# Kernel optimization log

Hardware: AMD Instinct MI355X
Metric: run time of the kernel (lower is better)

Reference implementation:

```python
import jax, jax.numpy as jnp
import numpy as np

INPUT_LEN = 24
HIDDEN = 64
BATCH = 8192


def _lstm_layer(seq, Wih, Whh, bih, bhh):
    """Single torch-style LSTM layer. seq: [T, B, in] -> hs: [T, B, H].
    Gate order matches torch: i, f, g, o."""
    B = seq.shape[1]
    H = Whh.shape[1]
    b = bih + bhh
    h0 = jnp.zeros((B, H), seq.dtype)
    c0 = jnp.zeros((B, H), seq.dtype)

    def step(carry, x_t):
        h, c = carry
        gates = x_t @ Wih.T + h @ Whh.T + b  # [B, 4H]
        i, f, g, o = jnp.split(gates, 4, axis=-1)
        c = jax.nn.sigmoid(f) * c + jax.nn.sigmoid(i) * jnp.tanh(g)
        h = jax.nn.sigmoid(o) * jnp.tanh(c)
        return (h, c), h

    _, hs = jax.lax.scan(step, (h0, c0), seq)
    return hs


def setup_inputs() -> dict:
    key = jax.random.key(0)
    ks = jax.random.split(key, 16)
    H = HIDDEN
    s = 1.0 / np.sqrt(H)  # torch LSTM/Linear init scale
    u = lambda k, shape, sc: jax.random.uniform(k, shape, jnp.float32, -sc, sc)
    return {
        "x": jax.random.normal(ks[0], (BATCH, INPUT_LEN), jnp.float32),
        # LSTM layer 0 (input size 1)
        "Wih0": u(ks[1], (4 * H, 1), s),
        "Whh0": u(ks[2], (4 * H, H), s),
        "bih0": u(ks[3], (4 * H,), s),
        "bhh0": u(ks[4], (4 * H,), s),
        # LSTM layer 1 (input size H)
        "Wih1": u(ks[5], (4 * H, H), s),
        "Whh1": u(ks[6], (4 * H, H), s),
        "bih1": u(ks[7], (4 * H,), s),
        "bhh1": u(ks[8], (4 * H,), s),
        # predictor MLP: Linear(H,32) -> ReLU -> Linear(32,1)
        "W1": u(ks[9], (32, H), s),
        "b1": u(ks[10], (32,), s),
        "W2": u(ks[11], (1, 32), 1.0 / np.sqrt(32)),
        "b2": u(ks[12], (1,), 1.0 / np.sqrt(32)),
        "damping": jnp.asarray(0.1, jnp.float32),
        "steps": 20,
    }


def reference(x, Wih0, Whh0, bih0, bhh0, Wih1, Whh1, bih1, bhh1,
              W1, b1, W2, b2, damping, steps):
    cur = x[..., None]  # [B, T, 1]
    alpha = jax.nn.sigmoid(damping)
    preds = []
    prev = None
    for _ in range(steps):
        seq = jnp.transpose(cur, (1, 0, 2))  # [T, B, 1]
        h1 = _lstm_layer(seq, Wih0, Whh0, bih0, bhh0)   # [T, B, H]
        h2 = _lstm_layer(h1, Wih1, Whh1, bih1, bhh1)     # [T, B, H]
        last = h2[-1]                                     # [B, H]
        pred = jax.nn.relu(last @ W1.T + b1) @ W2.T + b2  # [B, 1]
        if prev is not None:
            # torch: pred*(1-alpha) + predictions[-1].detach()*alpha*0.5
            pred = pred * (1.0 - alpha) + jax.lax.stop_gradient(prev) * alpha * 0.5
        preds.append(pred)
        prev = pred
        cur = jnp.concatenate([cur[:, 1:, :], pred[:, None, :]], axis=1)
    return jnp.concatenate(preds, axis=1)  # [B, steps]
```

## Files before the change

### kernel.cpp

```cpp
#include <hip/hip_runtime.h>


typedef _Float16 f16x8 __attribute__((ext_vector_type(8)));
typedef float f32x4 __attribute__((ext_vector_type(4)));

#define NBLK 512
#define NTHR 256
#define SRB  144

__device__ __forceinline__ float rcp_(float x) { return __builtin_amdgcn_rcpf(x); }
__device__ __forceinline__ float exp2_(float x) { return __builtin_amdgcn_exp2f(x); }
__device__ __forceinline__ f32x4 mfma16(uint4 a, uint4 b, f32x4 c) {
  return __builtin_amdgcn_mfma_f32_16x16x32_f16(
      __builtin_bit_cast(f16x8, a), __builtin_bit_cast(f16x8, b), c, 0, 0, 0);
}
__device__ __forceinline__ uint4 pack8s(const float* p, float s) {
  union { uint4 u; _Float16 h[8]; } r;
  #pragma unroll
  for (int i = 0; i < 8; ++i) r.h[i] = (_Float16)(p[i] * s);
  return r.u;
}
__device__ __forceinline__ float gatestep(float aI, float aF, float aG, float aO,
                                          float& cst) {
  float xx = exp2_(-aI), xf = exp2_(-aF), yy = exp2_(-aG), xo = exp2_(-aO);
  float P = (1.0f + xx) * (1.0f + yy);
  float Q = 1.0f + xf;
  float N = fmaf(cst, P, (1.0f - yy) * Q);
  float cv = N * rcp_(P * Q);
  cst = cv;
  float z = exp2_(-2.88539008178f * cv);
  return (1.0f - z) * rcp_((1.0f + xo) * (1.0f + z));
}

__global__ __launch_bounds__(NTHR, 2) void lstm_forecast(
    const float* __restrict__ x,
    const float* __restrict__ Wih0, const float* __restrict__ Whh0,
    const float* __restrict__ bih0, const float* __restrict__ bhh0,
    const float* __restrict__ Wih1, const float* __restrict__ Whh1,
    const float* __restrict__ bih1, const float* __restrict__ bhh1,
    const float* __restrict__ W1,   const float* __restrict__ b1,
    const float* __restrict__ W2,   const float* __restrict__ b2,
    const float* __restrict__ damping, const int* __restrict__ stepsPtr,
    float* __restrict__ out)
{
  __shared__ __align__(16) char h1s[2][16 * SRB];
  __shared__ __align__(16) char h2s[2][16 * SRB];
  __shared__ __align__(16) float win[24 * 16];
  __shared__ __align__(16) float pm[2][16];

  const int tid  = threadIdx.x;
  const int wave = tid >> 6;
  const int lane = tid & 63;
  const int cc   = lane & 15;
  const int hi   = lane >> 4;
  const int b0g  = blockIdx.x * 16;
  const float L2E = 1.44269504089f;

  uint4 wB0[4][2], wB1[4][2], wB2[4][2];
  float bias0v[4], wih0v[4];
  f32x4 bi1[4];
  #pragma unroll
  for (int gt = 0; gt < 4; ++gt) {
    float sc = (gt == 2) ? 2.0f * L2E : L2E;
    int row = (wave + 4 * gt) * 16 + cc;
    #pragma unroll
    for (int f = 0; f < 2; ++f) {
      int col = f * 32 + hi * 8;
      wB0[gt][f] = pack8s(Whh0 + row * 64 + col, sc);
      wB1[gt][f] = pack8s(Wih1 + row * 64 + col, sc);
      wB2[gt][f] = pack8s(Whh1 + row * 64 + col, sc);
    }
    bias0v[gt] = (bih0[row] + bhh0[row]) * sc;
    wih0v[gt]  = Wih0[row] * sc;
    float b1c  = (bih1[row] + bhh1[row]) * sc;
    #pragma unroll
    for (int r = 0; r < 4; ++r) bi1[gt][r] = b1c;
  }
  uint4 wM[2];
  {
    int row = (wave & 1) * 16 + cc;
    wM[0] = pack8s(W1 + row * 64 + hi * 8, 1.0f);
    wM[1] = pack8s(W1 + row * 64 + 32 + hi * 8, 1.0f);
  }
  const float w2v  = W2[(wave & 1) * 16 + cc];
  const float b1vv = b1[(wave & 1) * 16 + cc];
  const float alpha  = rcp_(1.0f + exp2_(-L2E * damping[0]));
  const int   nsteps = stepsPtr[0];
  const float b2v    = b2[0];

  for (int e = tid; e < 384; e += NTHR) {
    int b = e & 15, t = e >> 4;
    win[t * 16 + b] = x[(b0g + b) * 24 + t];
  }
  __syncthreads();

  const int offA = cc * SRB + hi * 16;
  const int offS = (wave * 16 + cc) * 2;
  float prevp = 0.0f;

  for (int s = 0; s < nsteps; ++s) {
    float c1[4] = {0, 0, 0, 0}, c2s[4] = {0, 0, 0, 0};

    {
      float4 xw = *(const float4*)&win[(s % 24) * 16 + hi * 4];
      float xa[4] = {xw.x, xw.y, xw.z, xw.w};
      #pragma unroll
      for (int r = 0; r < 4; ++r) {
        float hv = gatestep(fmaf(xa[r], wih0v[0], bias0v[0]),
                            fmaf(xa[r], wih0v[1], bias0v[1]),
                            fmaf(xa[r], wih0v[2], bias0v[2]),
                            fmaf(xa[r], wih0v[3], bias0v[3]), c1[r]);
        *(_Float16*)(h1s[0] + (hi * 4 + r) * SRB + offS) = (_Float16)hv;
      }
    }
    __syncthreads();
    uint4 a1lo = *(const uint4*)(h1s[0] + offA);
    uint4 a1hi = *(const uint4*)(h1s[0] + offA + 64);
    uint4 a2lo = make_uint4(0, 0, 0, 0), a2hi = make_uint4(0, 0, 0, 0);

    for (int t = 0; t < 23; ++t) {
      int pb = (t + 1) & 1;
      int ph = s + t + 1; if (ph >= 24) ph -= 24;
      float4 xw = *(const float4*)&win[ph * 16 + hi * 4];
      float xa[4] = {xw.x, xw.y, xw.z, xw.w};

      f32x4 acc1[4], acc0[4];
      #pragma unroll
      for (int gt = 0; gt < 4; ++gt) {
        f32x4 tv = mfma16(a1lo, wB1[gt][0], bi1[gt]);
        tv = mfma16(a1hi, wB1[gt][1], tv);
        tv = mfma16(a2lo, wB2[gt][0], tv);
        acc1[gt] = mfma16(a2hi, wB2[gt][1], tv);
      }
      #pragma unroll
      for (int gt = 0; gt < 4; ++gt) {
        f32x4 ai;
        #pragma unroll
        for (int r = 0; r < 4; ++r) ai[r] = fmaf(xa[r], wih0v[gt], bias0v[gt]);
        f32x4 tv = mfma16(a1lo, wB0[gt][0], ai);
        acc0[gt] = mfma16(a1hi, wB0[gt][1], tv);
      }

      char* h2d = h2s[pb];
      char* h1d = h1s[pb];
      #pragma unroll
      for (int r = 0; r < 4; ++r) {
        float hv = gatestep(acc1[0][r], acc1[1][r], acc1[2][r], acc1[3][r], c2s[r]);
        *(_Float16*)(h2d + (hi * 4 + r) * SRB + offS) = (_Float16)hv;
      }
      #pragma unroll
      for (int r = 0; r < 4; ++r) {
        float hv = gatestep(acc0[0][r], acc0[1][r], acc0[2][r], acc0[3][r], c1[r]);
        *(_Float16*)(h1d + (hi * 4 + r) * SRB + offS) = (_Float16)hv;
      }
      __syncthreads();
      a1lo = *(const uint4*)(h1s[pb] + offA);
      a1hi = *(const uint4*)(h1s[pb] + offA + 64);
      a2lo = *(const uint4*)(h2s[pb] + offA);
      a2hi = *(const uint4*)(h2s[pb] + offA + 64);
    }

    {
      f32x4 acc1[4];
      #pragma unroll
      for (int gt = 0; gt < 4; ++gt) {
        f32x4 tv = mfma16(a1lo, wB1[gt][0], bi1[gt]);
        tv = mfma16(a1hi, wB1[gt][1], tv);
        tv = mfma16(a2lo, wB2[gt][0], tv);
        acc1[gt] = mfma16(a2hi, wB2[gt][1], tv);
      }
      #pragma unroll
      for (int r = 0; r < 4; ++r) {
        float cv = c2s[r];
        float hv = gatestep(acc1[0][r], acc1[1][r], acc1[2][r], acc1[3][r], cv);
        *(_Float16*)(h2s[0] + (hi * 4 + r) * SRB + offS) = (_Float16)hv;
      }
    }
    __syncthreads();

    if (wave < 2) {
      uint4 hflo = *(const uint4*)(h2s[0] + offA);
      uint4 hfhi = *(const uint4*)(h2s[0] + offA + 64);
      f32x4 am;
      #pragma unroll
      for (int r = 0; r < 4; ++r) am[r] = b1vv;
      am = mfma16(hflo, wM[0], am);
      am = mfma16(hfhi, wM[1], am);
      float yp[4];
      #pragma unroll
      for (int r = 0; r < 4; ++r) yp[r] = fmaxf(am[r], 0.0f) * w2v;
      #pragma unroll
      for (int mask = 1; mask <= 8; mask <<= 1) {
        #pragma unroll
        for (int r = 0; r < 4; ++r) yp[r] += __shfl_xor(yp[r], mask);
      }
      if (cc == 0) {
        #pragma unroll
        for (int r = 0; r < 4; ++r) pm[wave][hi * 4 + r] = yp[r];
      }
    }
    __syncthreads();

    if (wave == 0 && lane < 16) {
      float y = pm[0][lane] + pm[1][lane] + b2v;
      float pd = (s == 0) ? y : fmaf(y, 1.0f - alpha, prevp * (alpha * 0.5f));
      prevp = pd;
      win[(s % 24) * 16 + lane] = pd;
      out[(long)(b0g + lane) * nsteps + s] = pd;
    }
    __syncthreads();
  }
}

extern "C" void kernel_launch(void* const* d_in, const int* in_sizes, int n_in,
                              void* d_out, int out_size, void* d_ws, size_t ws_size,
                              hipStream_t stream) {
  (void)in_sizes; (void)n_in; (void)out_size; (void)d_ws; (void)ws_size;
  lstm_forecast<<<NBLK, NTHR, 0, stream>>>(
      (const float*)d_in[0],
      (const float*)d_in[1],  (const float*)d_in[2],
      (const float*)d_in[3],  (const float*)d_in[4],
      (const float*)d_in[5],  (const float*)d_in[6],
      (const float*)d_in[7],  (const float*)d_in[8],
      (const float*)d_in[9],  (const float*)d_in[10],
      (const float*)d_in[11], (const float*)d_in[12],
      (const float*)d_in[13], (const int*)d_in[14],
      (float*)d_out);
}
```

Before: 597.0 us.

## Process two interleaved 16-row batch tiles per block to hide MFMA latency

Each block now handles 32 batch rows as two independent 16-row sub-tiles, interleaving their MFMA chains and gate computations inside one recurrence step. Half as many blocks are launched, with launch bounds lowered to one block per CU. The two independent dependency chains are meant to fill MFMA and transcendental latency inside a wave and to halve the barriers per unit of work. The cost is doubled register and LDS use per block and lower occupancy, which could spill registers or leave CUs underused.

```diff
diff --git a/kernel.cpp b/kernel.cpp
--- a/kernel.cpp
+++ b/kernel.cpp
@@ -4,7 +4,7 @@
 typedef _Float16 f16x8 __attribute__((ext_vector_type(8)));
 typedef float f32x4 __attribute__((ext_vector_type(4)));
 
-#define NBLK 512
+#define NBLK 256
 #define NTHR 256
 #define SRB  144
 
@@ -32,7 +32,7 @@
   return (1.0f - z) * rcp_((1.0f + xo) * (1.0f + z));
 }
 
-__global__ __launch_bounds__(NTHR, 2) void lstm_forecast(
+__global__ __launch_bounds__(NTHR, 1) void lstm_forecast(
     const float* __restrict__ x,
     const float* __restrict__ Wih0, const float* __restrict__ Whh0,
     const float* __restrict__ bih0, const float* __restrict__ bhh0,
@@ -43,17 +43,17 @@
     const float* __restrict__ damping, const int* __restrict__ stepsPtr,
     float* __restrict__ out)
 {
-  __shared__ __align__(16) char h1s[2][16 * SRB];
-  __shared__ __align__(16) char h2s[2][16 * SRB];
-  __shared__ __align__(16) float win[24 * 16];
-  __shared__ __align__(16) float pm[2][16];
+  __shared__ __align__(16) char h1s[2][2][16 * SRB];
+  __shared__ __align__(16) char h2s[2][2][16 * SRB];
+  __shared__ __align__(16) float win[2][24 * 16];
+  __shared__ __align__(16) float pm[2][2][16];
 
   const int tid  = threadIdx.x;
   const int wave = tid >> 6;
   const int lane = tid & 63;
   const int cc   = lane & 15;
   const int hi   = lane >> 4;
-  const int b0g  = blockIdx.x * 16;
+  const int b0g  = blockIdx.x * 32;
   const float L2E = 1.44269504089f;
 
   uint4 wB0[4][2], wB1[4][2], wB2[4][2];
@@ -88,99 +88,127 @@
   const int   nsteps = stepsPtr[0];
   const float b2v    = b2[0];
 
-  for (int e = tid; e < 384; e += NTHR) {
-    int b = e & 15, t = e >> 4;
-    win[t * 16 + b] = x[(b0g + b) * 24 + t];
+  for (int e = tid; e < 768; e += NTHR) {
+    int q   = (e >= 384) ? 1 : 0;
+    int rem = e - q * 384;
+    int b   = rem & 15, t = rem >> 4;
+    win[q][t * 16 + b] = x[(b0g + q * 16 + b) * 24 + t];
   }
   __syncthreads();
 
   const int offA = cc * SRB + hi * 16;
   const int offS = (wave * 16 + cc) * 2;
-  float prevp = 0.0f;
+  float prevp[2] = {0.0f, 0.0f};
 
   for (int s = 0; s < nsteps; ++s) {
-    float c1[4] = {0, 0, 0, 0}, c2s[4] = {0, 0, 0, 0};
-
-    {
-      float4 xw = *(const float4*)&win[(s % 24) * 16 + hi * 4];
+    float c1[2][4], c2s[2][4];
+    #pragma unroll
+    for (int q = 0; q < 2; ++q)
+      #pragma unroll
+      for (int r = 0; r < 4; ++r) { c1[q][r] = 0.0f; c2s[q][r] = 0.0f; }
+
+    #pragma unroll
+    for (int q = 0; q < 2; ++q) {
+      float4 xw = *(const float4*)&win[q][(s % 24) * 16 + hi * 4];
       float xa[4] = {xw.x, xw.y, xw.z, xw.w};
       #pragma unroll
       for (int r = 0; r < 4; ++r) {
         float hv = gatestep(fmaf(xa[r], wih0v[0], bias0v[0]),
                             fmaf(xa[r], wih0v[1], bias0v[1]),
                             fmaf(xa[r], wih0v[2], bias0v[2]),
-                            fmaf(xa[r], wih0v[3], bias0v[3]), c1[r]);
-        *(_Float16*)(h1s[0] + (hi * 4 + r) * SRB + offS) = (_Float16)hv;
-      }
-    }
-    __syncthreads();
-    uint4 a1lo = *(const uint4*)(h1s[0] + offA);
-    uint4 a1hi = *(const uint4*)(h1s[0] + offA + 64);
-    uint4 a2lo = make_uint4(0, 0, 0, 0), a2hi = make_uint4(0, 0, 0, 0);
+                            fmaf(xa[r], wih0v[3], bias0v[3]), c1[q][r]);
+        *(_Float16*)(h1s[q][0] + (hi * 4 + r) * SRB + offS) = (_Float16)hv;
+      }
+    }
+    __syncthreads();
+    uint4 a1lo[2], a1hi[2], a2lo[2], a2hi[2];
+    #pragma unroll
+    for (int q = 0; q < 2; ++q) {
+      a1lo[q] = *(const uint4*)(h1s[q][0] + offA);
+      a1hi[q] = *(const uint4*)(h1s[q][0] + offA + 64);
+      a2lo[q] = make_uint4(0, 0, 0, 0);
+      a2hi[q] = make_uint4(0, 0, 0, 0);
+    }
 
     for (int t = 0; t < 23; ++t) {
       int pb = (t + 1) & 1;
       int ph = s + t + 1; if (ph >= 24) ph -= 24;
-      float4 xw = *(const float4*)&win[ph * 16 + hi * 4];
-      float xa[4] = {xw.x, xw.y, xw.z, xw.w};
-
-      f32x4 acc1[4], acc0[4];
+
+      f32x4 acc1[2][4], acc0[2][4];
+      #pragma unroll
+      for (int q = 0; q < 2; ++q) {
+        #pragma unroll
+        for (int gt = 0; gt < 4; ++gt) {
+          f32x4 tv = mfma16(a1lo[q], wB1[gt][0], bi1[gt]);
+          tv = mfma16(a1hi[q], wB1[gt][1], tv);
+          tv = mfma16(a2lo[q], wB2[gt][0], tv);
+          acc1[q][gt] = mfma16(a2hi[q], wB2[gt][1], tv);
+        }
+      }
+      #pragma unroll
+      for (int q = 0; q < 2; ++q) {
+        float4 xw = *(const float4*)&win[q][ph * 16 + hi * 4];
+        float xa[4] = {xw.x, xw.y, xw.z, xw.w};
+        #pragma unroll
+        for (int gt = 0; gt < 4; ++gt) {
+          f32x4 ai;
+          #pragma unroll
+          for (int r = 0; r < 4; ++r) ai[r] = fmaf(xa[r], wih0v[gt], bias0v[gt]);
+          f32x4 tv = mfma16(a1lo[q], wB0[gt][0], ai);
+          acc0[q][gt] = mfma16(a1hi[q], wB0[gt][1], tv);
+        }
+      }
+
+      #pragma unroll
+      for (int q = 0; q < 2; ++q) {
+        char* h2d = h2s[q][pb];
+        char* h1d = h1s[q][pb];
+        #pragma unroll
+        for (int r = 0; r < 4; ++r) {
+          float hv = gatestep(acc1[q][0][r], acc1[q][1][r], acc1[q][2][r],
+                              acc1[q][3][r], c2s[q][r]);
+          *(_Float16*)(h2d + (hi * 4 + r) * SRB + offS) = (_Float16)hv;
+        }
+        #pragma unroll
+        for (int r = 0; r < 4; ++r) {
+          float hv = gatestep(acc0[q][0][r], acc0[q][1][r], acc0[q][2][r],
+                              acc0[q][3][r], c1[q][r]);
+          *(_Float16*)(h1d + (hi * 4 + r) * SRB + offS) = (_Float16)hv;
+        }
+      }
+      __syncthreads();
+      #pragma unroll
+      for (int q = 0; q < 2; ++q) {
+        a1lo[q] = *(const uint4*)(h1s[q][pb] + offA);
+        a1hi[q] = *(const uint4*)(h1s[q][pb] + offA + 64);
+        a2lo[q] = *(const uint4*)(h2s[q][pb] + offA);
+        a2hi[q] = *(const uint4*)(h2s[q][pb] + offA + 64);
+      }
+    }
+
+    #pragma unroll
+    for (int q = 0; q < 2; ++q) {
+      f32x4 acc1[4];
       #pragma unroll
       for (int gt = 0; gt < 4; ++gt) {
-        f32x4 tv = mfma16(a1lo, wB1[gt][0], bi1[gt]);
-        tv = mfma16(a1hi, wB1[gt][1], tv);
-        tv = mfma16(a2lo, wB2[gt][0], tv);
-        acc1[gt] = mfma16(a2hi, wB2[gt][1], tv);
-      }
-      #pragma unroll
-      for (int gt = 0; gt < 4; ++gt) {
-        f32x4 ai;
-        #pragma unroll
-        for (int r = 0; r < 4; ++r) ai[r] = fmaf(xa[r], wih0v[gt], bias0v[gt]);
-        f32x4 tv = mfma16(a1lo, wB0[gt][0], ai);
-        acc0[gt] = mfma16(a1hi, wB0[gt][1], tv);
-      }
-
-      char* h2d = h2s[pb];
-      char* h1d = h1s[pb];
+        f32x4 tv = mfma16(a1lo[q], wB1[gt][0], bi1[gt]);
+        tv = mfma16(a1hi[q], wB1[gt][1], tv);
+        tv = mfma16(a2lo[q], wB2[gt][0], tv);
+        acc1[gt] = mfma16(a2hi[q], wB2[gt][1], tv);
+      }
       #pragma unroll
       for (int r = 0; r < 4; ++r) {
-        float hv = gatestep(acc1[0][r], acc1[1][r], acc1[2][r], acc1[3][r], c2s[r]);
-        *(_Float16*)(h2d + (hi * 4 + r) * SRB + offS) = (_Float16)hv;
-      }
-      #pragma unroll
-      for (int r = 0; r < 4; ++r) {
-        float hv = gatestep(acc0[0][r], acc0[1][r], acc0[2][r], acc0[3][r], c1[r]);
-        *(_Float16*)(h1d + (hi * 4 + r) * SRB + offS) = (_Float16)hv;
-      }
-      __syncthreads();
-      a1lo = *(const uint4*)(h1s[pb] + offA);
-      a1hi = *(const uint4*)(h1s[pb] + offA + 64);
-      a2lo = *(const uint4*)(h2s[pb] + offA);
-      a2hi = *(const uint4*)(h2s[pb] + offA + 64);
-    }
+        float cv = c2s[q][r];
+        float hv = gatestep(acc1[0][r], acc1[1][r], acc1[2][r], acc1[3][r], cv);
+        *(_Float16*)(h2s[q][0] + (hi * 4 + r) * SRB + offS) = (_Float16)hv;
+      }
+    }
+    __syncthreads();
 
     {
-      f32x4 acc1[4];
-      #pragma unroll
-      for (int gt = 0; gt < 4; ++gt) {
-        f32x4 tv = mfma16(a1lo, wB1[gt][0], bi1[gt]);
-        tv = mfma16(a1hi, wB1[gt][1], tv);
-        tv = mfma16(a2lo, wB2[gt][0], tv);
-        acc1[gt] = mfma16(a2hi, wB2[gt][1], tv);
-      }
-      #pragma unroll
-      for (int r = 0; r < 4; ++r) {
-        float cv = c2s[r];
-        float hv = gatestep(acc1[0][r], acc1[1][r], acc1[2][r], acc1[3][r], cv);
-        *(_Float16*)(h2s[0] + (hi * 4 + r) * SRB + offS) = (_Float16)hv;
-      }
-    }
-    __syncthreads();
-
-    if (wave < 2) {
-      uint4 hflo = *(const uint4*)(h2s[0] + offA);
-      uint4 hfhi = *(const uint4*)(h2s[0] + offA + 64);
+      const int tq = wave >> 1;
+      uint4 hflo = *(const uint4*)(h2s[tq][0] + offA);
+      uint4 hfhi = *(const uint4*)(h2s[tq][0] + offA + 64);
       f32x4 am;
       #pragma unroll
       for (int r = 0; r < 4; ++r) am[r] = b1vv;
@@ -196,17 +224,23 @@
       }
       if (cc == 0) {
         #pragma unroll
-        for (int r = 0; r < 4; ++r) pm[wave][hi * 4 + r] = yp[r];
-      }
-    }
-    __syncthreads();
-
-    if (wave == 0 && lane < 16) {
-      float y = pm[0][lane] + pm[1][lane] + b2v;
-      float pd = (s == 0) ? y : fmaf(y, 1.0f - alpha, prevp * (alpha * 0.5f));
-      prevp = pd;
-      win[(s % 24) * 16 + lane] = pd;
-      out[(long)(b0g + lane) * nsteps + s] = pd;
+        for (int r = 0; r < 4; ++r) pm[tq][wave & 1][hi * 4 + r] = yp[r];
+      }
+    }
+    __syncthreads();
+
+    #pragma unroll
+    for (int q = 0; q < 2; ++q) {
+      if (lane < 16) {
+        float y = pm[q][0][lane] + pm[q][1][lane] + b2v;
+        float pd = (s == 0) ? y
+                            : fmaf(y, 1.0f - alpha, prevp[q] * (alpha * 0.5f));
+        prevp[q] = pd;
+        if (wave == 2 * q) {
+          win[q][(s % 24) * 16 + lane] = pd;
+          out[(long)(b0g + q * 16 + lane) * nsteps + s] = pd;
+        }
+      }
     }
     __syncthreads();
   }
```

After: 758.9 us. 1.27x slower.

## Defer MLP prediction head into next step's first timesteps to drop barriers

Applied to the files above, without the earlier changes.

Moves the per-step MLP head (predictor) out of the serial tail and overlaps it with the first LSTM timestep of the next forecast step. The window write and output store happen one timestep later, which removes two block-wide barriers per forecast step. The MLP weights move from registers into shared memory to cut register pressure, at the cost of extra LDS reads. The restructured loop needs a final epilogue for the last prediction, and its correctness depends on the window slot not being read before it is written.

```diff
diff --git a/kernel.cpp b/kernel.cpp
--- a/kernel.cpp
+++ b/kernel.cpp
@@ -47,6 +47,7 @@
   __shared__ __align__(16) char h2s[2][16 * SRB];
   __shared__ __align__(16) float win[24 * 16];
   __shared__ __align__(16) float pm[2][16];
+  __shared__ __align__(16) uint4 wfm[4][64];
 
   const int tid  = threadIdx.x;
   const int wave = tid >> 6;
@@ -76,11 +77,10 @@
     #pragma unroll
     for (int r = 0; r < 4; ++r) bi1[gt][r] = b1c;
   }
-  uint4 wM[2];
-  {
-    int row = (wave & 1) * 16 + cc;
-    wM[0] = pack8s(W1 + row * 64 + hi * 8, 1.0f);
-    wM[1] = pack8s(W1 + row * 64 + 32 + hi * 8, 1.0f);
+  for (int e = tid; e < 256; e += NTHR) {
+    int l = e & 63, f = (e >> 6) & 1, n = e >> 7;
+    wfm[n * 2 + f][l] =
+        pack8s(W1 + (n * 16 + (l & 15)) * 64 + f * 32 + (l >> 4) * 8, 1.0f);
   }
   const float w2v  = W2[(wave & 1) * 16 + cc];
   const float b1vv = b1[(wave & 1) * 16 + cc];
@@ -97,34 +97,119 @@
   const int offA = cc * SRB + hi * 16;
   const int offS = (wave * 16 + cc) * 2;
   float prevp = 0.0f;
+  float c1[4] = {0, 0, 0, 0}, c2s[4] = {0, 0, 0, 0};
+
+  {
+    float4 xw = *(const float4*)&win[0 * 16 + hi * 4];
+    float xa[4] = {xw.x, xw.y, xw.z, xw.w};
+    #pragma unroll
+    for (int r = 0; r < 4; ++r) {
+      float hv = gatestep(fmaf(xa[r], wih0v[0], bias0v[0]),
+                          fmaf(xa[r], wih0v[1], bias0v[1]),
+                          fmaf(xa[r], wih0v[2], bias0v[2]),
+                          fmaf(xa[r], wih0v[3], bias0v[3]), c1[r]);
+      *(_Float16*)(h1s[0] + (hi * 4 + r) * SRB + offS) = (_Float16)hv;
+    }
+  }
+  __syncthreads();
+  uint4 a1lo = *(const uint4*)(h1s[0] + offA);
+  uint4 a1hi = *(const uint4*)(h1s[0] + offA + 64);
+  uint4 a2lo = make_uint4(0, 0, 0, 0), a2hi = make_uint4(0, 0, 0, 0);
+  uint4 hflo = make_uint4(0, 0, 0, 0), hfhi = make_uint4(0, 0, 0, 0);
+
+#define CORE(PH, PB)                                                           \
+  do {                                                                         \
+    f32x4 acc1[4], acc0[4];                                                    \
+    _Pragma("unroll")                                                          \
+    for (int gt = 0; gt < 4; ++gt) {                                           \
+      f32x4 tv = mfma16(a1lo, wB1[gt][0], bi1[gt]);                            \
+      tv = mfma16(a1hi, wB1[gt][1], tv);                                       \
+      tv = mfma16(a2lo, wB2[gt][0], tv);                                       \
+      acc1[gt] = mfma16(a2hi, wB2[gt][1], tv);                                 \
+    }                                                                          \
+    float4 xw = *(const float4*)&win[(PH) * 16 + hi * 4];                      \
+    float xa[4] = {xw.x, xw.y, xw.z, xw.w};                                    \
+    _Pragma("unroll")                                                          \
+    for (int gt = 0; gt < 4; ++gt) {                                           \
+      f32x4 ai;                                                                \
+      _Pragma("unroll")                                                        \
+      for (int r = 0; r < 4; ++r) ai[r] = fmaf(xa[r], wih0v[gt], bias0v[gt]);  \
+      f32x4 tv = mfma16(a1lo, wB0[gt][0], ai);                                 \
+      acc0[gt] = mfma16(a1hi, wB0[gt][1], tv);                                 \
+    }                                                                          \
+    _Pragma("unroll")                                                          \
+    for (int r = 0; r < 4; ++r) {                                              \
+      float hv = gatestep(acc1[0][r], acc1[1][r], acc1[2][r], acc1[3][r],      \
+                          c2s[r]);                                             \
+      *(_Float16*)(h2s[PB] + (hi * 4 + r) * SRB + offS) = (_Float16)hv;        \
+    }                                                                          \
+    _Pragma("unroll")                                                          \
+    for (int r = 0; r < 4; ++r) {                                              \
+      float hv = gatestep(acc0[0][r], acc0[1][r], acc0[2][r], acc0[3][r],      \
+                          c1[r]);                                              \
+      *(_Float16*)(h1s[PB] + (hi * 4 + r) * SRB + offS) = (_Float16)hv;        \
+    }                                                                          \
+  } while (0)
+
+#define LOADFRAGS(PB)                                                          \
+  do {                                                                         \
+    a1lo = *(const uint4*)(h1s[PB] + offA);                                    \
+    a1hi = *(const uint4*)(h1s[PB] + offA + 64);                               \
+    a2lo = *(const uint4*)(h2s[PB] + offA);                                    \
+    a2hi = *(const uint4*)(h2s[PB] + offA + 64);                               \
+  } while (0)
 
   for (int s = 0; s < nsteps; ++s) {
-    float c1[4] = {0, 0, 0, 0}, c2s[4] = {0, 0, 0, 0};
-
     {
-      float4 xw = *(const float4*)&win[(s % 24) * 16 + hi * 4];
-      float xa[4] = {xw.x, xw.y, xw.z, xw.w};
-      #pragma unroll
-      for (int r = 0; r < 4; ++r) {
-        float hv = gatestep(fmaf(xa[r], wih0v[0], bias0v[0]),
-                            fmaf(xa[r], wih0v[1], bias0v[1]),
-                            fmaf(xa[r], wih0v[2], bias0v[2]),
-                            fmaf(xa[r], wih0v[3], bias0v[3]), c1[r]);
-        *(_Float16*)(h1s[0] + (hi * 4 + r) * SRB + offS) = (_Float16)hv;
-      }
-    }
-    __syncthreads();
-    uint4 a1lo = *(const uint4*)(h1s[0] + offA);
-    uint4 a1hi = *(const uint4*)(h1s[0] + offA + 64);
-    uint4 a2lo = make_uint4(0, 0, 0, 0), a2hi = make_uint4(0, 0, 0, 0);
-
-    for (int t = 0; t < 23; ++t) {
+      int ph = s + 1; if (ph >= 24) ph -= 24;
+      CORE(ph, 1);
+      if (s > 0 && wave < 2) {
+        uint4 m0 = wfm[(wave & 1) * 2 + 0][lane];
+        uint4 m1 = wfm[(wave & 1) * 2 + 1][lane];
+        f32x4 am;
+        #pragma unroll
+        for (int r = 0; r < 4; ++r) am[r] = b1vv;
+        am = mfma16(hflo, m0, am);
+        am = mfma16(hfhi, m1, am);
+        float yp[4];
+        #pragma unroll
+        for (int r = 0; r < 4; ++r) yp[r] = fmaxf(am[r], 0.0f) * w2v;
+        #pragma unroll
+        for (int mask = 1; mask <= 8; mask <<= 1) {
+          #pragma unroll
+          for (int r = 0; r < 4; ++r) yp[r] += __shfl_xor(yp[r], mask);
+        }
+        if (cc == 0) {
+          #pragma unroll
+          for (int r = 0; r < 4; ++r) pm[wave][hi * 4 + r] = yp[r];
+        }
+      }
+      __syncthreads();
+      LOADFRAGS(1);
+    }
+    {
+      if (s > 0 && wave == 0 && lane < 16) {
+        float y = pm[0][lane] + pm[1][lane] + b2v;
+        float pd = (s == 1) ? y : fmaf(y, 1.0f - alpha, prevp * (alpha * 0.5f));
+        prevp = pd;
+        int slot = (s - 1) % 24;
+        win[slot * 16 + lane] = pd;
+        out[(long)(b0g + lane) * nsteps + (s - 1)] = pd;
+      }
+      int ph = s + 2; if (ph >= 24) ph -= 24;
+      CORE(ph, 0);
+      __syncthreads();
+      LOADFRAGS(0);
+    }
+    for (int t = 2; t < 23; ++t) {
       int pb = (t + 1) & 1;
       int ph = s + t + 1; if (ph >= 24) ph -= 24;
-      float4 xw = *(const float4*)&win[ph * 16 + hi * 4];
-      float xa[4] = {xw.x, xw.y, xw.z, xw.w};
-
-      f32x4 acc1[4], acc0[4];
+      CORE(ph, pb);
+      __syncthreads();
+      LOADFRAGS(pb);
+    }
+    {
+      f32x4 acc1[4];
       #pragma unroll
       for (int gt = 0; gt < 4; ++gt) {
         f32x4 tv = mfma16(a1lo, wB1[gt][0], bi1[gt]);
@@ -133,83 +218,66 @@
         acc1[gt] = mfma16(a2hi, wB2[gt][1], tv);
       }
       #pragma unroll
-      for (int gt = 0; gt < 4; ++gt) {
-        f32x4 ai;
-        #pragma unroll
-        for (int r = 0; r < 4; ++r) ai[r] = fmaf(xa[r], wih0v[gt], bias0v[gt]);
-        f32x4 tv = mfma16(a1lo, wB0[gt][0], ai);
-        acc0[gt] = mfma16(a1hi, wB0[gt][1], tv);
-      }
-
-      char* h2d = h2s[pb];
-      char* h1d = h1s[pb];
-      #pragma unroll
       for (int r = 0; r < 4; ++r) {
-        float hv = gatestep(acc1[0][r], acc1[1][r], acc1[2][r], acc1[3][r], c2s[r]);
-        *(_Float16*)(h2d + (hi * 4 + r) * SRB + offS) = (_Float16)hv;
-      }
-      #pragma unroll
-      for (int r = 0; r < 4; ++r) {
-        float hv = gatestep(acc0[0][r], acc0[1][r], acc0[2][r], acc0[3][r], c1[r]);
-        *(_Float16*)(h1d + (hi * 4 + r) * SRB + offS) = (_Float16)hv;
-      }
-      __syncthreads();
-      a1lo = *(const uint4*)(h1s[pb] + offA);
-      a1hi = *(const uint4*)(h1s[pb] + offA + 64);
-      a2lo = *(const uint4*)(h2s[pb] + offA);
-      a2hi = *(const uint4*)(h2s[pb] + offA + 64);
-    }
-
-    {
-      f32x4 acc1[4];
-      #pragma unroll
-      for (int gt = 0; gt < 4; ++gt) {
-        f32x4 tv = mfma16(a1lo, wB1[gt][0], bi1[gt]);
-        tv = mfma16(a1hi, wB1[gt][1], tv);
-        tv = mfma16(a2lo, wB2[gt][0], tv);
-        acc1[gt] = mfma16(a2hi, wB2[gt][1], tv);
-      }
-      #pragma unroll
-      for (int r = 0; r < 4; ++r) {
-        float cv = c2s[r];
-        float hv = gatestep(acc1[0][r], acc1[1][r], acc1[2][r], acc1[3][r], cv);
+        float hv = gatestep(acc1[0][r], acc1[1][r], acc1[2][r], acc1[3][r],
+                            c2s[r]);
         *(_Float16*)(h2s[0] + (hi * 4 + r) * SRB + offS) = (_Float16)hv;
       }
-    }
-    __syncthreads();
-
-    if (wave < 2) {
-      uint4 hflo = *(const uint4*)(h2s[0] + offA);
-      uint4 hfhi = *(const uint4*)(h2s[0] + offA + 64);
-      f32x4 am;
-      #pragma unroll
-      for (int r = 0; r < 4; ++r) am[r] = b1vv;
-      am = mfma16(hflo, wM[0], am);
-      am = mfma16(hfhi, wM[1], am);
-      float yp[4];
-      #pragma unroll
-      for (int r = 0; r < 4; ++r) yp[r] = fmaxf(am[r], 0.0f) * w2v;
-      #pragma unroll
-      for (int mask = 1; mask <= 8; mask <<= 1) {
-        #pragma unroll
-        for (int r = 0; r < 4; ++r) yp[r] += __shfl_xor(yp[r], mask);
-      }
-      if (cc == 0) {
-        #pragma unroll
-        for (int r = 0; r < 4; ++r) pm[wave][hi * 4 + r] = yp[r];
-      }
-    }
-    __syncthreads();
-
-    if (wave == 0 && lane < 16) {
-      float y = pm[0][lane] + pm[1][lane] + b2v;
-      float pd = (s == 0) ? y : fmaf(y, 1.0f - alpha, prevp * (alpha * 0.5f));
-      prevp = pd;
-      win[(s % 24) * 16 + lane] = pd;
-      out[(long)(b0g + lane) * nsteps + s] = pd;
-    }
-    __syncthreads();
-  }
+      if (s < nsteps - 1) {
+        int ph = s + 1; if (ph >= 24) ph -= 24;
+        float4 xw = *(const float4*)&win[ph * 16 + hi * 4];
+        float xa[4] = {xw.x, xw.y, xw.z, xw.w};
+        #pragma unroll
+        for (int r = 0; r < 4; ++r) {
+          c1[r] = 0.0f;
+          float hv = gatestep(fmaf(xa[r], wih0v[0], bias0v[0]),
+                              fmaf(xa[r], wih0v[1], bias0v[1]),
+                              fmaf(xa[r], wih0v[2], bias0v[2]),
+                              fmaf(xa[r], wih0v[3], bias0v[3]), c1[r]);
+          *(_Float16*)(h1s[0] + (hi * 4 + r) * SRB + offS) = (_Float16)hv;
+        }
+      }
+      #pragma unroll
+      for (int r = 0; r < 4; ++r) c2s[r] = 0.0f;
+      __syncthreads();
+      a1lo = *(const uint4*)(h1s[0] + offA);
+      a1hi = *(const uint4*)(h1s[0] + offA + 64);
+      a2lo = make_uint4(0, 0, 0, 0);
+      a2hi = make_uint4(0, 0, 0, 0);
+      hflo = *(const uint4*)(h2s[0] + offA);
+      hfhi = *(const uint4*)(h2s[0] + offA + 64);
+    }
+  }
+
+  if (wave < 2) {
+    uint4 m0 = wfm[(wave & 1) * 2 + 0][lane];
+    uint4 m1 = wfm[(wave & 1) * 2 + 1][lane];
+    f32x4 am;
+    #pragma unroll
+    for (int r = 0; r < 4; ++r) am[r] = b1vv;
+    am = mfma16(hflo, m0, am);
+    am = mfma16(hfhi, m1, am);
+    float yp[4];
+    #pragma unroll
+    for (int r = 0; r < 4; ++r) yp[r] = fmaxf(am[r], 0.0f) * w2v;
+    #pragma unroll
+    for (int mask = 1; mask <= 8; mask <<= 1) {
+      #pragma unroll
+      for (int r = 0; r < 4; ++r) yp[r] += __shfl_xor(yp[r], mask);
+    }
+    if (cc == 0) {
+      #pragma unroll
+      for (int r = 0; r < 4; ++r) pm[wave][hi * 4 + r] = yp[r];
+    }
+  }
+  __syncthreads();
+  if (wave == 0 && lane < 16) {
+    float y = pm[0][lane] + pm[1][lane] + b2v;
+    float pd = (nsteps == 1) ? y : fmaf(y, 1.0f - alpha, prevp * (alpha * 0.5f));
+    out[(long)(b0g + lane) * nsteps + (nsteps - 1)] = pd;
+  }
+#undef CORE
+#undef LOADFRAGS
 }
 
 extern "C" void kernel_launch(void* const* d_in, const int* in_sizes, int n_in,
```

Result: slower. 628.7 us (+5.3%).

## Interleave consecutive forecast steps to halve barriers and overlap recurrences

Applied to the files above, without the earlier changes.

Restructures the step loop so the second half of step b's LSTM recurrence runs alongside the first half of step b+1's. This works because step b+1's early timesteps only need window values that are already known. Each barrier now serves two independent recurrence chains, which roughly halves the barrier count per forecast step and adds instruction-level parallelism. The MLP head and the blend of step b's prediction are slotted into the early iterations of the next block. The cost is double-buffered shared state for two steps in flight. The barrier between loading the input window and the first prologue was also dropped, which risks a shared-memory race.

```diff
diff --git a/kernel.cpp b/kernel.cpp
--- a/kernel.cpp
+++ b/kernel.cpp
@@ -43,8 +43,8 @@
     const float* __restrict__ damping, const int* __restrict__ stepsPtr,
     float* __restrict__ out)
 {
-  __shared__ __align__(16) char h1s[2][16 * SRB];
-  __shared__ __align__(16) char h2s[2][16 * SRB];
+  __shared__ __align__(16) char h1s[2][2][16 * SRB];
+  __shared__ __align__(16) char h2s[2][2][16 * SRB];
   __shared__ __align__(16) float win[24 * 16];
   __shared__ __align__(16) float pm[2][16];
 
@@ -92,46 +92,56 @@
     int b = e & 15, t = e >> 4;
     win[t * 16 + b] = x[(b0g + b) * 24 + t];
   }
-  __syncthreads();
 
   const int offA = cc * SRB + hi * 16;
   const int offS = (wave * 16 + cc) * 2;
   float prevp = 0.0f;
-
-  for (int s = 0; s < nsteps; ++s) {
-    float c1[4] = {0, 0, 0, 0}, c2s[4] = {0, 0, 0, 0};
-
-    {
-      float4 xw = *(const float4*)&win[(s % 24) * 16 + hi * 4];
-      float xa[4] = {xw.x, xw.y, xw.z, xw.w};
-      #pragma unroll
-      for (int r = 0; r < 4; ++r) {
-        float hv = gatestep(fmaf(xa[r], wih0v[0], bias0v[0]),
-                            fmaf(xa[r], wih0v[1], bias0v[1]),
-                            fmaf(xa[r], wih0v[2], bias0v[2]),
-                            fmaf(xa[r], wih0v[3], bias0v[3]), c1[r]);
-        *(_Float16*)(h1s[0] + (hi * 4 + r) * SRB + offS) = (_Float16)hv;
-      }
-    }
-    __syncthreads();
-    uint4 a1lo = *(const uint4*)(h1s[0] + offA);
-    uint4 a1hi = *(const uint4*)(h1s[0] + offA + 64);
-    uint4 a2lo = make_uint4(0, 0, 0, 0), a2hi = make_uint4(0, 0, 0, 0);
-
-    for (int t = 0; t < 23; ++t) {
-      int pb = (t + 1) & 1;
-      int ph = s + t + 1; if (ph >= 24) ph -= 24;
+  float cX1[4], cX2[4], cY1[4], cY2[4];
+
+  auto prologue = [&](int s2, char* h1c0, float* c1) {
+    int ph = s2; if (ph >= 24) ph -= 24;
+    float4 xw = *(const float4*)&win[ph * 16 + hi * 4];
+    float xa[4] = {xw.x, xw.y, xw.z, xw.w};
+    #pragma unroll
+    for (int r = 0; r < 4; ++r) {
+      c1[r] = 0.0f;
+      float hv = gatestep(fmaf(xa[r], wih0v[0], bias0v[0]),
+                          fmaf(xa[r], wih0v[1], bias0v[1]),
+                          fmaf(xa[r], wih0v[2], bias0v[2]),
+                          fmaf(xa[r], wih0v[3], bias0v[3]), c1[r]);
+      *(_Float16*)(h1c0 + (hi * 4 + r) * SRB + offS) = (_Float16)hv;
+    }
+  };
+
+  auto core = [&](int s, int it, char* h1c0, char* h1c1, char* h2c0, char* h2c1,
+                  float* c1, float* c2, bool last) {
+    const bool rp = (it & 1) != 0;
+    char* h1r = rp ? h1c1 : h1c0;
+    char* h2r = rp ? h2c1 : h2c0;
+    char* h1w = rp ? h1c0 : h1c1;
+    char* h2w = rp ? h2c0 : h2c1;
+    uint4 a1lo = *(const uint4*)(h1r + offA);
+    uint4 a1hi = *(const uint4*)(h1r + offA + 64);
+    uint4 a2lo, a2hi;
+    if (it == 0) {
+      a2lo = make_uint4(0, 0, 0, 0); a2hi = a2lo;
+    } else {
+      a2lo = *(const uint4*)(h2r + offA);
+      a2hi = *(const uint4*)(h2r + offA + 64);
+    }
+    f32x4 acc1[4];
+    #pragma unroll
+    for (int gt = 0; gt < 4; ++gt) {
+      f32x4 tv = mfma16(a1lo, wB1[gt][0], bi1[gt]);
+      tv = mfma16(a1hi, wB1[gt][1], tv);
+      tv = mfma16(a2lo, wB2[gt][0], tv);
+      acc1[gt] = mfma16(a2hi, wB2[gt][1], tv);
+    }
+    if (!last) {
+      int ph = s + it + 1; if (ph >= 24) ph -= 24;
       float4 xw = *(const float4*)&win[ph * 16 + hi * 4];
       float xa[4] = {xw.x, xw.y, xw.z, xw.w};
-
-      f32x4 acc1[4], acc0[4];
-      #pragma unroll
-      for (int gt = 0; gt < 4; ++gt) {
-        f32x4 tv = mfma16(a1lo, wB1[gt][0], bi1[gt]);
-        tv = mfma16(a1hi, wB1[gt][1], tv);
-        tv = mfma16(a2lo, wB2[gt][0], tv);
-        acc1[gt] = mfma16(a2hi, wB2[gt][1], tv);
-      }
+      f32x4 acc0[4];
       #pragma unroll
       for (int gt = 0; gt < 4; ++gt) {
         f32x4 ai;
@@ -140,47 +150,29 @@
         f32x4 tv = mfma16(a1lo, wB0[gt][0], ai);
         acc0[gt] = mfma16(a1hi, wB0[gt][1], tv);
       }
-
-      char* h2d = h2s[pb];
-      char* h1d = h1s[pb];
       #pragma unroll
       for (int r = 0; r < 4; ++r) {
-        float hv = gatestep(acc1[0][r], acc1[1][r], acc1[2][r], acc1[3][r], c2s[r]);
-        *(_Float16*)(h2d + (hi * 4 + r) * SRB + offS) = (_Float16)hv;
+        float hv = gatestep(acc1[0][r], acc1[1][r], acc1[2][r], acc1[3][r], c2[r]);
+        *(_Float16*)(h2w + (hi * 4 + r) * SRB + offS) = (_Float16)hv;
       }
       #pragma unroll
       for (int r = 0; r < 4; ++r) {
         float hv = gatestep(acc0[0][r], acc0[1][r], acc0[2][r], acc0[3][r], c1[r]);
-        *(_Float16*)(h1d + (hi * 4 + r) * SRB + offS) = (_Float16)hv;
-      }
-      __syncthreads();
-      a1lo = *(const uint4*)(h1s[pb] + offA);
-      a1hi = *(const uint4*)(h1s[pb] + offA + 64);
-      a2lo = *(const uint4*)(h2s[pb] + offA);
-      a2hi = *(const uint4*)(h2s[pb] + offA + 64);
-    }
-
-    {
-      f32x4 acc1[4];
-      #pragma unroll
-      for (int gt = 0; gt < 4; ++gt) {
-        f32x4 tv = mfma16(a1lo, wB1[gt][0], bi1[gt]);
-        tv = mfma16(a1hi, wB1[gt][1], tv);
-        tv = mfma16(a2lo, wB2[gt][0], tv);
-        acc1[gt] = mfma16(a2hi, wB2[gt][1], tv);
-      }
+        *(_Float16*)(h1w + (hi * 4 + r) * SRB + offS) = (_Float16)hv;
+      }
+    } else {
       #pragma unroll
       for (int r = 0; r < 4; ++r) {
-        float cv = c2s[r];
-        float hv = gatestep(acc1[0][r], acc1[1][r], acc1[2][r], acc1[3][r], cv);
-        *(_Float16*)(h2s[0] + (hi * 4 + r) * SRB + offS) = (_Float16)hv;
-      }
-    }
-    __syncthreads();
-
+        float hv = gatestep(acc1[0][r], acc1[1][r], acc1[2][r], acc1[3][r], c2[r]);
+        *(_Float16*)(h2w + (hi * 4 + r) * SRB + offS) = (_Float16)hv;
+      }
+    }
+  };
+
+  auto mlp = [&](char* h2c0) {
     if (wave < 2) {
-      uint4 hflo = *(const uint4*)(h2s[0] + offA);
-      uint4 hfhi = *(const uint4*)(h2s[0] + offA + 64);
+      uint4 hflo = *(const uint4*)(h2c0 + offA);
+      uint4 hfhi = *(const uint4*)(h2c0 + offA + 64);
       f32x4 am;
       #pragma unroll
       for (int r = 0; r < 4; ++r) am[r] = b1vv;
@@ -199,17 +191,59 @@
         for (int r = 0; r < 4; ++r) pm[wave][hi * 4 + r] = yp[r];
       }
     }
-    __syncthreads();
-
+  };
+
+  auto blend = [&](int sPred, bool writeWin) {
     if (wave == 0 && lane < 16) {
       float y = pm[0][lane] + pm[1][lane] + b2v;
-      float pd = (s == 0) ? y : fmaf(y, 1.0f - alpha, prevp * (alpha * 0.5f));
+      float pd = (sPred == 0) ? y : fmaf(y, 1.0f - alpha, prevp * (alpha * 0.5f));
       prevp = pd;
-      win[(s % 24) * 16 + lane] = pd;
-      out[(long)(b0g + lane) * nsteps + s] = pd;
-    }
-    __syncthreads();
-  }
+      if (writeWin) {
+        int slot = sPred; if (slot >= 24) slot -= 24;
+        win[slot * 16 + lane] = pd;
+      }
+      out[(long)(b0g + lane) * nsteps + sPred] = pd;
+    }
+  };
+
+  auto blockBody = [&](int b,
+                       float* c1A, float* c2A, char* h1A0, char* h1A1,
+                       char* h2A0, char* h2A1,
+                       float* c1B, float* c2B, char* h1B0, char* h1B1,
+                       char* h2B0, char* h2B1) {
+    const bool hasA = (b >= 0);
+    const bool hasB = (b + 1 < nsteps);
+    for (int t = 0; t < 12; ++t) {
+      if (hasA) core(b, t + 12, h1A0, h1A1, h2A0, h2A1, c1A, c2A, t == 11);
+      if (hasB) core(b + 1, t, h1B0, h1B1, h2B0, h2B1, c1B, c2B, false);
+      if (t == 0 && b >= 1) mlp(h2B0);
+      if (t == 1 && b >= 1) blend(b - 1, true);
+      if (t == 11 && b + 2 < nsteps) {
+        prologue(b + 2, h1A0, c1A);
+        #pragma unroll
+        for (int r = 0; r < 4; ++r) c2A[r] = 0.0f;
+      }
+      __syncthreads();
+    }
+  };
+
+  prologue(0, h1s[0][0], cX1);
+  #pragma unroll
+  for (int r = 0; r < 4; ++r) cX2[r] = 0.0f;
+  __syncthreads();
+
+  for (int b = -1; b < nsteps; ++b) {
+    if ((b & 1) == 0)
+      blockBody(b, cX1, cX2, h1s[0][0], h1s[0][1], h2s[0][0], h2s[0][1],
+                   cY1, cY2, h1s[1][0], h1s[1][1], h2s[1][0], h2s[1][1]);
+    else
+      blockBody(b, cY1, cY2, h1s[1][0], h1s[1][1], h2s[1][0], h2s[1][1],
+                   cX1, cX2, h1s[0][0], h1s[0][1], h2s[0][0], h2s[0][1]);
+  }
+
+  mlp(h2s[(nsteps - 1) & 1][0]);
+  __syncthreads();
+  blend(nsteps - 1, false);
 }
 
 extern "C" void kernel_launch(void* const* d_in, const int* in_sizes, int n_in,
```

Result: slower. 633.4 us (+6.1%).
